# Performance work log

Measured on AMD Instinct MI355X. Metric: run time of the kernel, lower is better.

The kernel has to match this reference:

```python
import jax, jax.numpy as jnp
import numpy as np

FLOAT_MAX = 3.4e38
FLOAT_MIN = -3.4e38


def _net1_forward(link_mtx, action_mask, col_table, rel_table, graph_weight,
                  graph_bias, Wk, Wq, Wv, fc_w, table_ids, l_col_ids, r_col_ids):
    emb = rel_table.shape[1]

    # ---- graph_forward: GCN layer over relation graph, mean pooling ----
    # link_mtx: [B, R, R], rel_table: [R, E]
    support = jnp.einsum('bnm,me->bne', link_mtx, rel_table)          # [B, R, E]
    out_graph = jax.nn.relu(support @ graph_weight + graph_bias)      # [B, R, G]
    pooled = out_graph.mean(axis=1)                                   # [B, G]

    # ---- tree_forward: batched left-deep join trees via scan over depth ----
    # table_ids: [B, T, D+1]; col ids: [B, T, D, C]
    r_tabs = rel_table[table_ids[..., 1:]]                            # [B, T, D, E]
    l_cols = col_table[l_col_ids].mean(axis=-2)                       # [B, T, D, E] (mean pooling of joined cols)
    r_cols = col_table[r_col_ids].mean(axis=-2)                       # [B, T, D, E]
    xs = (jnp.moveaxis(r_tabs, 2, 0), jnp.moveaxis(l_cols, 2, 0),
          jnp.moveaxis(r_cols, 2, 0))                                  # each [D, B, T, E]
    init = rel_table[table_ids[..., 0]]                               # [B, T, E] leftmost leaf

    def step(prev, x):
        rte, lce, rce = x
        # query_emb = cat([l_table, l_col, r_col, r_table]) -> 4 tokens
        q = jnp.stack([prev, lce, rce, rte], axis=-2)                 # [B, T, 4, E]
        K = q @ Wk
        Q = q @ Wq
        V = q @ Wv
        scores = jnp.einsum('btqe,btke->btqk', Q, K) / emb            # note: /emb, not /sqrt(emb)
        attn = jax.nn.softmax(scores, axis=-1)
        out = jnp.einsum('btqk,btke->btqe', attn, V).sum(axis=-2)     # sum over query rows -> [B, T, E]
        return out, None

    final, _ = jax.lax.scan(step, init, xs)                           # [B, T, E]
    tree_emb = final.sum(axis=1)                                      # sum over subtrees -> [B, E]

    logits = jnp.concatenate([pooled, tree_emb], axis=1) @ fc_w       # [B, A]
    inf_mask = jnp.clip(jnp.log(action_mask), FLOAT_MIN, FLOAT_MAX)
    return inf_mask + logits


def setup_inputs() -> dict:
    key = jax.random.key(0)
    ks = jax.random.split(key, 12)
    B, T, D, C = 8, 8, 16, 2
    num_rel, num_col, num_actions = 4096, 20000, 4096
    emb, gdim = 64, 64
    std = 0.05
    return {
        'link_mtx': jax.random.uniform(ks[0], (B, num_rel, num_rel), dtype=jnp.float32),
        'action_mask': jnp.ones((B, num_actions), dtype=jnp.float32),
        'col_table': jax.random.normal(ks[1], (num_col, emb), dtype=jnp.float32) * std,
        'rel_table': jax.random.normal(ks[2], (num_rel, emb), dtype=jnp.float32) * std,
        'graph_weight': jax.random.normal(ks[3], (emb, gdim), dtype=jnp.float32) * std,
        'graph_bias': jnp.zeros((gdim,), dtype=jnp.float32),
        'Wk': jax.random.normal(ks[4], (emb, emb), dtype=jnp.float32) * std,
        'Wq': jax.random.normal(ks[5], (emb, emb), dtype=jnp.float32) * std,
        'Wv': jax.random.normal(ks[6], (emb, emb), dtype=jnp.float32) * std,
        'fc_w': jax.random.normal(ks[7], (gdim + emb, num_actions), dtype=jnp.float32) * std,
        'table_ids': jax.random.randint(ks[8], (B, T, D + 1), 0, num_rel),
        'l_col_ids': jax.random.randint(ks[9], (B, T, D, C), 0, num_col),
        'r_col_ids': jax.random.randint(ks[10], (B, T, D, C), 0, num_col),
    }


def reference(link_mtx, action_mask, col_table, rel_table, graph_weight,
              graph_bias, Wk, Wq, Wv, fc_w, table_ids, l_col_ids, r_col_ids):
    return _net1_forward(link_mtx, action_mask, col_table, rel_table, graph_weight,
                         graph_bias, Wk, Wq, Wv, fc_w, table_ids, l_col_ids, r_col_ids)
```

## Files before the change

### kernel.cpp

```cpp
#include <hip/hip_runtime.h>
#include <hip/hip_bf16.h>
#include <stdint.h>

typedef __attribute__((ext_vector_type(8))) short short8;
typedef __attribute__((ext_vector_type(4))) float f32x4;

union FragU { short8 s; __hip_bfloat162 h[4]; };
union BU { uint4 u; short8 s; };

__device__ __forceinline__ unsigned short f2bf(float f) {
  union { float f; unsigned int u; } v; v.f = f;
  unsigned int r = v.u + 0x7fffu + ((v.u >> 16) & 1u);
  return (unsigned short)(r >> 16);
}
__device__ __forceinline__ float bf2f(unsigned short h) {
  union { unsigned int u; float f; } v; v.u = ((unsigned int)h) << 16;
  return v.f;
}

#define GLOAD_LDS16(gp, lp) \
  __builtin_amdgcn_global_load_lds((const __attribute__((address_space(1))) void*)(gp), \
                                   (__attribute__((address_space(3))) void*)(lp), 16, 0, 0)

__global__ void k_prep(const float* __restrict__ rel, const float* __restrict__ GW,
                       unsigned short* __restrict__ bTf, float* __restrict__ accums) {
  __shared__ float tile[64][65];
  __shared__ float gws[64][64];
  __shared__ float relgw[64][64];
  const int j = blockIdx.x;
  const int t = threadIdx.x;
#pragma unroll
  for (int p = 0; p < 16; ++p) {
    int elem = p * 256 + t;
    int kk = elem >> 6, ee = elem & 63;
    tile[kk][ee] = rel[(j * 64 + kk) * 64 + ee];
    ((float*)gws)[elem] = GW[elem];
  }
  __syncthreads();
  {
    const int e = t >> 2, chunk = t & 3;
    for (int i = 0; i < 16; ++i) {
      float acc = 0.f;
#pragma unroll
      for (int ii = 0; ii < 64; ++ii) acc += tile[chunk * 16 + i][ii] * gws[ii][e];
      relgw[chunk * 16 + i][e] = acc;
    }
  }
  __syncthreads();
#pragma unroll
  for (int m = 0; m < 2; ++m) {
    const int f = t * 2 + m;
    const int nt = f >> 7, kc = (f >> 6) & 1, ln = f & 63;
    const int g = ln >> 4, r = ln & 15;
    union { unsigned short u16[8]; uint4 v; } pk;
#pragma unroll
    for (int s = 0; s < 8; ++s) pk.u16[s] = f2bf(relgw[kc * 32 + g * 8 + s][nt * 16 + r]);
    *(uint4*)(bTf + (size_t)j * 4096 + f * 8) = pk.v;
  }
  if (j == 0) {
    accums[t] = 0.f; accums[t + 256] = 0.f; accums[t + 512] = 0.f; accums[t + 768] = 0.f;
  }
}

__global__ __launch_bounds__(256, 3) void k_main(
    const float* __restrict__ link, const unsigned short* __restrict__ bTf,
    const float* __restrict__ gbias, float* __restrict__ pooled_sum,
    const float* __restrict__ col_table, const float* __restrict__ rel_table,
    const float* __restrict__ Wk, const float* __restrict__ Wq, const float* __restrict__ Wv,
    const int* __restrict__ table_ids, const int* __restrict__ l_ids,
    const int* __restrict__ r_ids, float* __restrict__ tree_emb) {
  __shared__ union {
    struct { char a[4][2][4096]; } g;
    struct { unsigned short W3b[3 * 4096]; float qT[4][64][4]; } tr;
  } sm;

  const int t = threadIdx.x;
  const int lane = t & 63;
  const int wid = t >> 6;

  if (blockIdx.x >= 16) {
    const int gid = blockIdx.x - 16;
    const int b = gid >> 6;
    const int rb = gid & 63;
    const int rowG0 = rb * 64 + wid * 16;
    const int phase = (gid * 4 + wid + b * 9) & 63;
    const int g = lane >> 4;
    const int r = lane & 15;
    const uint32_t fr = (uint32_t)((r & 7) << 4);

    const char* linkb = (const char*)(link + ((size_t)b << 24));
    const char* bTfb = (const char*)bTf;
    const int a_ri = lane >> 4;
    const uint32_t a_cb = (uint32_t)((lane & 15) * 16);

    char* a0buf = sm.g.a[wid][0];
    char* a1buf = sm.g.a[wid][1];

    f32x4 acc[4];
#pragma unroll
    for (int nt = 0; nt < 4; ++nt) acc[nt] = (f32x4){0.f, 0.f, 0.f, 0.f};
    uint4 bq[8];

#define STAGEA(ab_, tta) do {                                              \
    const size_t ka = (size_t)(tta) * 256;                                 \
    _Pragma("unroll")                                                      \
    for (int j = 0; j < 4; ++j) {                                          \
      const int wlrow = 4 * j + a_ri;                                      \
      const uint32_t cb = a_cb ^ ((uint32_t)(wlrow & 7) << 4);             \
      GLOAD_LDS16(linkb + (size_t)(rowG0 + wlrow) * 16384 + ka + cb,       \
                  (ab_) + j * 1024);                                       \
    }                                                                      \
  } while (0)

#define LOADB(tta) do {                                                    \
    const char* bb = bTfb + (size_t)(tta) * 8192 + lane * 16;              \
    _Pragma("unroll")                                                      \
    for (int j = 0; j < 8; ++j) bq[j] = *(const uint4*)(bb + j * 1024);    \
  } while (0)

#define COMPUTEW(ab_) do {                                                 \
    const char* ar = (ab_) + r * 256;                                      \
    _Pragma("unroll")                                                      \
    for (int kc = 0; kc < 2; ++kc) {                                       \
      const uint32_t o0 = ((uint32_t)(kc * 128 + g * 32)) ^ fr;            \
      const f32x4 a0 = *(const f32x4*)(ar + o0);                           \
      const f32x4 a1 = *(const f32x4*)(ar + (o0 ^ 16));                    \
      FragU f;                                                             \
      f.h[0] = __float22bfloat162_rn(float2{a0[0], a0[1]});                \
      f.h[1] = __float22bfloat162_rn(float2{a0[2], a0[3]});                \
      f.h[2] = __float22bfloat162_rn(float2{a1[0], a1[1]});                \
      f.h[3] = __float22bfloat162_rn(float2{a1[2], a1[3]});                \
      _Pragma("unroll")                                                    \
      for (int nt = 0; nt < 4; ++nt) {                                     \
        BU bu; bu.u = bq[nt * 2 + kc];                                     \
        acc[nt] = __builtin_amdgcn_mfma_f32_16x16x32_bf16(f.s, bu.s, acc[nt], 0, 0, 0); \
      }                                                                    \
    }                                                                      \
  } while (0)

    STAGEA(a0buf, phase);
    for (int it2 = 0; it2 < 32; ++it2) {
      const int te = 2 * it2, to = te + 1;
      LOADB((te + phase) & 63);
      asm volatile("" ::: "memory");
      STAGEA(a1buf, (te + 1 + phase) & 63);
      asm volatile("s_waitcnt vmcnt(4)" ::: "memory");
      COMPUTEW(a0buf);
      LOADB((to + phase) & 63);
      asm volatile("" ::: "memory");
      if (it2 < 31) {
        STAGEA(a0buf, (to + 1 + phase) & 63);
        asm volatile("s_waitcnt vmcnt(4)" ::: "memory");
      } else {
        asm volatile("s_waitcnt vmcnt(0)" ::: "memory");
      }
      COMPUTEW(a1buf);
    }

#pragma unroll
    for (int nt = 0; nt < 4; ++nt) {
      const float gbv = gbias[nt * 16 + r];
      float s = 0.f;
#pragma unroll
      for (int j = 0; j < 4; ++j) s += fmaxf(acc[nt][j] + gbv, 0.f);
      s += __shfl_xor(s, 16);
      s += __shfl_xor(s, 32);
      if (g == 0) atomicAdd(&pooled_sum[b * 64 + nt * 16 + r], s);
    }
  } else {
    const int e = lane;
    for (int i = t; i < 3 * 4096; i += 256) {
      float v;
      if (i < 4096) v = Wk[i];
      else if (i < 8192) v = Wq[i - 4096];
      else v = Wv[i - 8192];
      sm.tr.W3b[i] = f2bf(v);
    }
    __syncthreads();

    const int tree = blockIdx.x * 4 + wid;
    const int b = tree >> 3;
    const int* tid = table_ids + tree * 17;
    const int* lid = l_ids + tree * 32;
    const int* rid = r_ids + tree * 32;

    float prev = rel_table[tid[0] * 64 + e];

    for (int d = 0; d < 16; ++d) {
      const int l0 = lid[d * 2], l1 = lid[d * 2 + 1];
      const int r0 = rid[d * 2], r1 = rid[d * 2 + 1];
      const float lce = 0.5f * (col_table[l0 * 64 + e] + col_table[l1 * 64 + e]);
      const float rce = 0.5f * (col_table[r0 * 64 + e] + col_table[r1 * 64 + e]);
      const float rte = rel_table[tid[1 + d] * 64 + e];
      float4 qv0; qv0.x = prev; qv0.y = lce; qv0.z = rce; qv0.w = rte;
      *(float4*)&sm.tr.qT[wid][e][0] = qv0;
      __syncthreads();

      float K[4] = {0, 0, 0, 0}, Q[4] = {0, 0, 0, 0}, V[4] = {0, 0, 0, 0};
#pragma unroll 8
      for (int i = 0; i < 64; ++i) {
        const f32x4 qv = *(const f32x4*)&sm.tr.qT[wid][i][0];
        const float wk = bf2f(sm.tr.W3b[i * 64 + e]);
        const float wq = bf2f(sm.tr.W3b[4096 + i * 64 + e]);
        const float wvv = bf2f(sm.tr.W3b[8192 + i * 64 + e]);
#pragma unroll
        for (int j = 0; j < 4; ++j) {
          K[j] += qv[j] * wk;
          Q[j] += qv[j] * wq;
          V[j] += qv[j] * wvv;
        }
      }

      float sc[4][4];
#pragma unroll
      for (int j = 0; j < 4; ++j)
#pragma unroll
        for (int k = 0; k < 4; ++k) {
          float p = Q[j] * K[k];
          p += __shfl_xor(p, 1);  p += __shfl_xor(p, 2);  p += __shfl_xor(p, 4);
          p += __shfl_xor(p, 8);  p += __shfl_xor(p, 16); p += __shfl_xor(p, 32);
          sc[j][k] = p * (1.f / 64.f);
        }

      float wsum[4] = {0, 0, 0, 0};
#pragma unroll
      for (int j = 0; j < 4; ++j) {
        float mx = fmaxf(fmaxf(sc[j][0], sc[j][1]), fmaxf(sc[j][2], sc[j][3]));
        float a0 = __expf(sc[j][0] - mx), a1 = __expf(sc[j][1] - mx);
        float a2 = __expf(sc[j][2] - mx), a3 = __expf(sc[j][3] - mx);
        float inv = 1.f / (a0 + a1 + a2 + a3);
        wsum[0] += a0 * inv; wsum[1] += a1 * inv; wsum[2] += a2 * inv; wsum[3] += a3 * inv;
      }

      prev = wsum[0] * V[0] + wsum[1] * V[1] + wsum[2] * V[2] + wsum[3] * V[3];
      __syncthreads();
    }
    atomicAdd(&tree_emb[b * 64 + e], prev);
  }
}

__global__ void k_final(const float* __restrict__ action_mask, const float* __restrict__ fc_w,
                        const float* __restrict__ pooled_sum, const float* __restrict__ tree_emb,
                        float* __restrict__ out) {
  __shared__ float c[128];
  const int b = blockIdx.x >> 4;
  const int a = ((blockIdx.x & 15) << 8) + threadIdx.x;
  if (threadIdx.x < 128) {
    c[threadIdx.x] = (threadIdx.x < 64) ? pooled_sum[b * 64 + threadIdx.x] * (1.f / 4096.f)
                                        : tree_emb[b * 64 + threadIdx.x - 64];
  }
  __syncthreads();
  float acc = 0.f;
  for (int i = 0; i < 128; ++i) acc += c[i] * fc_w[i * 4096 + a];
  const float m = action_mask[b * 4096 + a];
  float lg = __logf(m);
  lg = fminf(fmaxf(lg, -3.4e38f), 3.4e38f);
  out[b * 4096 + a] = lg + acc;
}

extern "C" void kernel_launch(void* const* d_in, const int* in_sizes, int n_in,
                              void* d_out, int out_size, void* d_ws, size_t ws_size,
                              hipStream_t stream) {
  const float* link = (const float*)d_in[0];
  const float* mask = (const float*)d_in[1];
  const float* col = (const float*)d_in[2];
  const float* rel = (const float*)d_in[3];
  const float* GW = (const float*)d_in[4];
  const float* gb = (const float*)d_in[5];
  const float* Wk = (const float*)d_in[6];
  const float* Wq = (const float*)d_in[7];
  const float* Wv = (const float*)d_in[8];
  const float* fcw = (const float*)d_in[9];
  const int* tids = (const int*)d_in[10];
  const int* lids = (const int*)d_in[11];
  const int* rids = (const int*)d_in[12];
  float* out = (float*)d_out;

  unsigned short* bTf = (unsigned short*)d_ws;
  float* accums = (float*)((char*)d_ws + 512 * 1024);
  float* pooled_sum = accums;
  float* tree = accums + 512;

  hipLaunchKernelGGL(k_prep, dim3(64), dim3(256), 0, stream, rel, GW, bTf, accums);
  hipLaunchKernelGGL(k_main, dim3(528), dim3(256), 0, stream,
                     link, bTf, gb, pooled_sum,
                     col, rel, Wk, Wq, Wv, tids, lids, rids, tree);
  hipLaunchKernelGGL(k_final, dim3(128), dim3(256), 0, stream, mask, fcw, pooled_sum, tree, out);
}
```

Measured before the change: 150.5 us.

## Deepen GCN link-matrix pipeline with double-buffered B fragments and two-stage prefetch

The main GEMM loop now keeps two register buffers for the B fragments and prefetches both the next two A tiles (global-to-LDS) and B tiles before computing, waiting with vmcnt(12) so one full stage stays in flight during each compute. This aims to hide global-load latency better than the previous one-stage lookahead. To make room for the extra registers, the launch bound drops from 3 to 2 blocks per CU, which reduces occupancy and the latency hiding that comes from running more waves.

```diff
diff --git a/kernel.cpp b/kernel.cpp
--- a/kernel.cpp
+++ b/kernel.cpp
@@ -62,7 +62,7 @@
   }
 }
 
-__global__ __launch_bounds__(256, 3) void k_main(
+__global__ __launch_bounds__(256, 2) void k_main(
     const float* __restrict__ link, const unsigned short* __restrict__ bTf,
     const float* __restrict__ gbias, float* __restrict__ pooled_sum,
     const float* __restrict__ col_table, const float* __restrict__ rel_table,
@@ -99,7 +99,7 @@
     f32x4 acc[4];
 #pragma unroll
     for (int nt = 0; nt < 4; ++nt) acc[nt] = (f32x4){0.f, 0.f, 0.f, 0.f};
-    uint4 bq[8];
+    uint4 bq0[8], bq1[8];
 
 #define STAGEA(ab_, tta) do {                                              \
     const size_t ka = (size_t)(tta) * 256;                                 \
@@ -112,13 +112,13 @@
     }                                                                      \
   } while (0)
 
-#define LOADB(tta) do {                                                    \
+#define LOADB(bq_, tta) do {                                               \
     const char* bb = bTfb + (size_t)(tta) * 8192 + lane * 16;              \
     _Pragma("unroll")                                                      \
-    for (int j = 0; j < 8; ++j) bq[j] = *(const uint4*)(bb + j * 1024);    \
+    for (int j = 0; j < 8; ++j) bq_[j] = *(const uint4*)(bb + j * 1024);   \
   } while (0)
 
-#define COMPUTEW(ab_) do {                                                 \
+#define COMPUTEW(ab_, bq_) do {                                            \
     const char* ar = (ab_) + r * 256;                                      \
     _Pragma("unroll")                                                      \
     for (int kc = 0; kc < 2; ++kc) {                                       \
@@ -132,29 +132,32 @@
       f.h[3] = __float22bfloat162_rn(float2{a1[2], a1[3]});                \
       _Pragma("unroll")                                                    \
       for (int nt = 0; nt < 4; ++nt) {                                     \
-        BU bu; bu.u = bq[nt * 2 + kc];                                     \
+        BU bu; bu.u = bq_[nt * 2 + kc];                                    \
         acc[nt] = __builtin_amdgcn_mfma_f32_16x16x32_bf16(f.s, bu.s, acc[nt], 0, 0, 0); \
       }                                                                    \
     }                                                                      \
   } while (0)
 
     STAGEA(a0buf, phase);
+    LOADB(bq0, phase);
+    STAGEA(a1buf, (phase + 1) & 63);
+    LOADB(bq1, (phase + 1) & 63);
+
     for (int it2 = 0; it2 < 32; ++it2) {
-      const int te = 2 * it2, to = te + 1;
-      LOADB((te + phase) & 63);
-      asm volatile("" ::: "memory");
-      STAGEA(a1buf, (te + 1 + phase) & 63);
-      asm volatile("s_waitcnt vmcnt(4)" ::: "memory");
-      COMPUTEW(a0buf);
-      LOADB((to + phase) & 63);
-      asm volatile("" ::: "memory");
+      const int te = 2 * it2;
+      asm volatile("s_waitcnt vmcnt(12)" ::: "memory");
+      COMPUTEW(a0buf, bq0);
       if (it2 < 31) {
-        STAGEA(a0buf, (to + 1 + phase) & 63);
-        asm volatile("s_waitcnt vmcnt(4)" ::: "memory");
-      } else {
-        asm volatile("s_waitcnt vmcnt(0)" ::: "memory");
-      }
-      COMPUTEW(a1buf);
+        STAGEA(a0buf, (te + 2 + phase) & 63);
+        LOADB(bq0, (te + 2 + phase) & 63);
+      }
+      if (it2 < 31) { asm volatile("s_waitcnt vmcnt(12)" ::: "memory"); }
+      else          { asm volatile("s_waitcnt vmcnt(0)"  ::: "memory"); }
+      COMPUTEW(a1buf, bq1);
+      if (it2 < 31) {
+        STAGEA(a1buf, (te + 3 + phase) & 63);
+        LOADB(bq1, (te + 3 + phase) & 63);
+      }
     }
 
 #pragma unroll
```

Result: no change. 150.9 us (+0.3%).
